# Kernel tuning notes

Hardware: AMD Instinct MI355X
Metric: run time of the kernel (lower is better)

## Reference

```python
import jax, jax.numpy as jnp
import numpy as np

B, S, D, H, FF = 16, 1024, 1024, 8, 4096
DH = D // H
EPS = 1e-5

def _ln(x, g, b):
    mu = jnp.mean(x, axis=-1, keepdims=True)
    var = jnp.mean((x - mu) ** 2, axis=-1, keepdims=True)
    return (x - mu) * jax.lax.rsqrt(var + EPS) * g + b

def setup_inputs() -> dict:
    key = jax.random.key(0)
    ks = jax.random.split(key, 12)
    sd = D ** -0.5
    return {
        "x": jax.random.normal(ks[0], (B, S, D), jnp.float32),
        "bias": jax.random.normal(ks[1], (S, S), jnp.float32),
        "Wq": jax.random.normal(ks[2], (D, D), jnp.float32) * sd,
        "bq": jnp.zeros((D,), jnp.float32),
        "Wk": jax.random.normal(ks[3], (D, D), jnp.float32) * sd,
        "bk": jnp.zeros((D,), jnp.float32),
        "Wv": jax.random.normal(ks[4], (D, D), jnp.float32) * sd,
        "bv": jnp.zeros((D,), jnp.float32),
        "Wo": jax.random.normal(ks[5], (D, D), jnp.float32) * sd,
        "bo": jnp.zeros((D,), jnp.float32),
        "ln1_g": jnp.ones((D,), jnp.float32),
        "ln1_b": jnp.zeros((D,), jnp.float32),
        "W1": jax.random.normal(ks[6], (FF, D), jnp.float32) * sd,
        "b1": jnp.zeros((FF,), jnp.float32),
        "W2": jax.random.normal(ks[7], (D, FF), jnp.float32) * (FF ** -0.5),
        "b2": jnp.zeros((D,), jnp.float32),
        "ln2_g": jnp.ones((D,), jnp.float32),
        "ln2_b": jnp.zeros((D,), jnp.float32),
    }

def reference(x, bias, Wq, bq, Wk, bk, Wv, bv, Wo, bo, ln1_g, ln1_b,
              W1, b1, W2, b2, ln2_g, ln2_b):
    # torch nn.Linear: y = x @ W.T + b
    Q = x @ Wq.T + bq  # [B,S,D]
    K = x @ Wk.T + bk
    V = x @ Wv.T + bv
    # Faithful to torch: plain row-major reshape [B,S,H*dh] -> [B*H,S,dh]
    Q = Q.reshape(B * H, S, DH)
    K = K.reshape(B * H, S, DH)
    V = V.reshape(B * H, S, DH)
    scale = DH ** -0.5
    scores = jnp.einsum('bqd,bkd->bqk', Q, K)  # [B*H,S,S]
    scores = (scores + bias[None]) * scale      # bias added BEFORE scaling, as in source
    attn = jax.nn.softmax(scores, axis=-1)
    selfattention = attn[0]
    ctx = jnp.einsum('bqk,bkd->bqd', attn, V).reshape(B, S, D)
    out = ctx @ Wo.T + bo
    out = _ln(out + x, ln1_g, ln1_b)
    # FFN
    h = jax.nn.relu(out @ W1.T + b1)
    ff = h @ W2.T + b2
    out2 = _ln(ff + out, ln2_g, ln2_b)
    return out2, selfattention
```

## Files before the change

### kernel.cpp

```cpp
#include <hip/hip_runtime.h>
#include <hip/hip_bf16.h>
#include <math.h>

typedef __attribute__((ext_vector_type(4))) float f32x4;
typedef __attribute__((ext_vector_type(8))) __bf16 bf16x8;
typedef __attribute__((ext_vector_type(4))) __bf16 bf16x4;

static constexpr float SCALE = 0.08838834764831845f;

__device__ __forceinline__ void load_lds16(const void* g, void* l) {
  __builtin_amdgcn_global_load_lds(
      (const __attribute__((address_space(1))) void*)g,
      (__attribute__((address_space(3))) void*)l, 16, 0, 0);
}

__global__ __launch_bounds__(256) void cast_kernel(const float* __restrict__ s,
                                                   __bf16* __restrict__ d, int n4) {
  int i = blockIdx.x * blockDim.x + threadIdx.x;
  int stride = gridDim.x * blockDim.x;
  for (; i < n4; i += stride) {
    float4 v = reinterpret_cast<const float4*>(s)[i];
    bf16x4 o;
    o[0] = (__bf16)v.x; o[1] = (__bf16)v.y; o[2] = (__bf16)v.z; o[3] = (__bf16)v.w;
    reinterpret_cast<bf16x4*>(d)[i] = o;
  }
}

__global__ __launch_bounds__(256) void transpose_bias(const float* __restrict__ src,
                                                      __bf16* __restrict__ dst) {
  __shared__ float tile[64][65];
  const int bx = blockIdx.x & 15;
  const int by = blockIdx.x >> 4;
  const int t = threadIdx.x;
  const int lx = t & 63, ly = t >> 6;
#pragma unroll
  for (int i = 0; i < 16; ++i) {
    int row = (ly << 4) + i;
    tile[row][lx] = src[(size_t)(by * 64 + row) * 1024 + bx * 64 + lx];
  }
  __syncthreads();
#pragma unroll
  for (int i = 0; i < 16; ++i) {
    int row = (ly << 4) + i;
    dst[(size_t)(bx * 64 + row) * 1024 + by * 64 + lx] = (__bf16)tile[lx][row];
  }
}

template <int EPI>
__global__ __launch_bounds__(512, 2) void gemm_bt(
    const __bf16* __restrict__ A, const __bf16* __restrict__ Bw,
    const float* __restrict__ bvec, __bf16* __restrict__ Cb,
    float* __restrict__ Cf, int M, int N, int K) {
  __shared__ __align__(16) char sm[131072];

  const int ntn = N >> 8;
  const int nwg = gridDim.x;
  const int bid = blockIdx.x;
  const int b = (bid & 7) * (nwg >> 3) + (bid >> 3);
  const int tm = b / ntn, tn = b % ntn;
  const int t = threadIdx.x, lane = t & 63;
  const int w = t >> 6;
  const int wm = w >> 2, wn = w & 3;
  const int l15 = lane & 15, lq = lane >> 4;

  f32x4 acc[8][4] = {};

  const int r0 = t >> 3;
  const int r1 = r0 + 64;
  const int kb0 = (((t & 7) << 4) ^ ((r0 & 7) << 4));
  const int wbase = w << 10;

  auto stage = [&](int kt, int p) {
    char* base = sm + (p << 16);
    const size_t kofs = (size_t)(kb0 >> 1) + ((size_t)kt << 6);
#pragma unroll
    for (int h = 0; h < 2; ++h) {
      const __bf16* gA = A + (size_t)((tm << 8) + (h << 7) + r0) * K + kofs;
      const __bf16* gA2 = A + (size_t)((tm << 8) + (h << 7) + r1) * K + kofs;
      char* lA = base + (h << 14) + wbase;
      load_lds16(gA, lA);
      load_lds16(gA2, lA + 8192);
      const __bf16* gB = Bw + (size_t)((tn << 8) + (h << 7) + r0) * K + kofs;
      const __bf16* gB2 = Bw + (size_t)((tn << 8) + (h << 7) + r1) * K + kofs;
      char* lB = base + 32768 + (h << 14) + wbase;
      load_lds16(gB, lB);
      load_lds16(gB2, lB + 8192);
    }
  };

  stage(0, 0);
  __syncthreads();

  const int NT = K >> 6;
  const int rbB = (wn & 1) << 6;
  for (int kt = 0; kt < NT; ++kt) {
    const int p = kt & 1;
    const char* Ab = sm + (p << 16) + (wm << 14);
    const char* Bb = sm + (p << 16) + 32768 + ((wn >> 1) << 14);
    if (kt + 1 < NT) stage(kt + 1, p ^ 1);

    bf16x8 bfv[4][2];
#pragma unroll
    for (int nf = 0; nf < 4; ++nf) {
      const int r = rbB + (nf << 4) + l15;
      const int sw = (r & 7) << 4;
#pragma unroll
      for (int ks = 0; ks < 2; ++ks) {
        const int lb = (ks << 6) + (lq << 4);
        bfv[nf][ks] = *(const bf16x8*)(Bb + r * 128 + (lb ^ sw));
      }
    }
#pragma unroll
    for (int q = 0; q < 4; ++q) {
      bf16x8 af[2][2];
#pragma unroll
      for (int dm = 0; dm < 2; ++dm) {
        const int r = (((q << 1) + dm) << 4) + l15;
        const int sw = (r & 7) << 4;
#pragma unroll
        for (int ks = 0; ks < 2; ++ks) {
          const int lb = (ks << 6) + (lq << 4);
          af[dm][ks] = *(const bf16x8*)(Ab + r * 128 + (lb ^ sw));
        }
      }
#pragma unroll
      for (int ks = 0; ks < 2; ++ks)
#pragma unroll
        for (int dm = 0; dm < 2; ++dm)
#pragma unroll
          for (int nf = 0; nf < 4; ++nf)
            acc[(q << 1) + dm][nf] = __builtin_amdgcn_mfma_f32_16x16x32_bf16(
                af[dm][ks], bfv[nf][ks], acc[(q << 1) + dm][nf], 0, 0, 0);
    }
    __syncthreads();
  }

  const int row0 = (tm << 8) + (wm << 7) + (lq << 2);
  const int col0 = (tn << 8) + (wn << 6) + l15;
#pragma unroll
  for (int nf = 0; nf < 4; ++nf) {
    const int col = col0 + (nf << 4);
    const float bv = bvec[col];
#pragma unroll
    for (int mf = 0; mf < 8; ++mf) {
#pragma unroll
      for (int r = 0; r < 4; ++r) {
        const int row = row0 + (mf << 4) + r;
        float v = acc[mf][nf][r] + bv;
        if (EPI == 1) v = fmaxf(v, 0.f);
        if (EPI == 2) {
          Cf[(size_t)row * N + col] = v;
        } else if (EPI == 3) {
          size_t vt = ((size_t)(row >> 7) << 17) + ((size_t)(col & 127) << 10) +
                      ((row & 127) << 3) + (col >> 7);
          Cb[vt] = (__bf16)v;
        } else {
          Cb[(size_t)row * N + col] = (__bf16)v;
        }
      }
    }
  }
}

__global__ __launch_bounds__(256) void attn_flash(
    const __bf16* __restrict__ Q, const __bf16* __restrict__ K,
    const __bf16* __restrict__ VT, const __bf16* __restrict__ biasT,
    __bf16* __restrict__ ctx) {
  __shared__ __bf16 Qs[64 * 128];
  __shared__ __bf16 Ks[64 * 128];
  __shared__ __bf16 VTs[128 * 64];
  __shared__ __bf16 Ps[4][16 * 64];

  const int bid = blockIdx.x;
  const int b = ((bid & 7) << 8) | (bid >> 3);
  const int g = b >> 4;
  const int q0 = (b & 15) << 6;
  const size_t goff = (size_t)g << 17;
  const __bf16* Qg = Q + goff;
  const __bf16* Kg = K + goff;
  const __bf16* VTg = VT + goff;

  const int t = threadIdx.x, w = t >> 6, lane = t & 63;
  const int l15 = lane & 15, lq = lane >> 4;

  {
    int srow = lane >> 4;
    int sbo = (lane & 15) << 4;
#pragma unroll
    for (int i = 0; i < 4; ++i) {
      int c = (w << 2) + i;
      int r = (c << 2) + srow;
      int ke = (sbo ^ ((r & 7) << 4)) >> 1;
      load_lds16(Qg + (size_t)(q0 + r) * 128 + ke, (char*)Qs + (c << 10));
    }
  }

  float mrun = -INFINITY, lrun = 0.f;
  f32x4 cacc[8] = {};
  bf16x8 qf[4];
  const int qg = q0 + (w << 4) + l15;
  const int ra = (w << 4) + l15;

  for (int kb = 0; kb < 1024; kb += 64) {
    {
      int srow = lane >> 4;
      int sbo = (lane & 15) << 4;
#pragma unroll
      for (int i = 0; i < 4; ++i) {
        int c = (w << 2) + i;
        int r = (c << 2) + srow;
        int ke = (sbo ^ ((r & 7) << 4)) >> 1;
        load_lds16(Kg + (size_t)(kb + r) * 128 + ke, (char*)Ks + (c << 10));
      }
    }
    {
      int srow = lane >> 3;
      int sbo = (lane & 7) << 4;
#pragma unroll
      for (int i = 0; i < 4; ++i) {
        int c = (w << 2) + i;
        int e = (c << 3) + srow;
        int ke = kb + ((sbo ^ ((e & 7) << 4)) >> 1);
        load_lds16(VTg + (size_t)e * 1024 + ke, (char*)VTs + (c << 10));
      }
    }
    __syncthreads();

    if (kb == 0) {
#pragma unroll
      for (int ec = 0; ec < 4; ++ec) {
        int lb = (ec << 6) + (lq << 4);
        qf[ec] = *(const bf16x8*)((const char*)Qs + ra * 256 + (lb ^ ((ra & 7) << 4)));
      }
    }

    f32x4 sacc[4] = {};
#pragma unroll
    for (int ec = 0; ec < 4; ++ec) {
      const int lb = (ec << 6) + (lq << 4);
#pragma unroll
      for (int kn = 0; kn < 4; ++kn) {
        int rb = (kn << 4) + l15;
        bf16x8 kf = *(const bf16x8*)((const char*)Ks + rb * 256 + (lb ^ ((rb & 7) << 4)));
        sacc[kn] = __builtin_amdgcn_mfma_f32_16x16x32_bf16(kf, qf[ec], sacc[kn], 0, 0, 0);
      }
    }

    float sv[4][4];
#pragma unroll
    for (int kn = 0; kn < 4; ++kn) {
      int kbase = kb + (kn << 4) + (lq << 2);
#pragma unroll
      for (int r = 0; r < 4; ++r)
        sv[kn][r] = (sacc[kn][r] + (float)biasT[((size_t)(kbase + r) << 10) + qg]) * SCALE;
    }
    float mt = sv[0][0];
#pragma unroll
    for (int kn = 0; kn < 4; ++kn)
#pragma unroll
      for (int r = 0; r < 4; ++r) mt = fmaxf(mt, sv[kn][r]);
    mt = fmaxf(mt, __shfl_xor(mt, 16));
    mt = fmaxf(mt, __shfl_xor(mt, 32));
    float mnew = fmaxf(mrun, mt);
    float alpha = __expf(mrun - mnew);
    mrun = mnew;
    float psum = 0.f;
#pragma unroll
    for (int kn = 0; kn < 4; ++kn)
#pragma unroll
      for (int r = 0; r < 4; ++r) {
        float p = __expf(sv[kn][r] - mnew);
        sv[kn][r] = p;
        psum += p;
      }
    psum += __shfl_xor(psum, 16);
    psum += __shfl_xor(psum, 32);
    lrun = lrun * alpha + psum;

    float alphaR[4];
#pragma unroll
    for (int r = 0; r < 4; ++r)
      alphaR[r] = __shfl(alpha, (lane & 48) + ((lane & 48) >> 2) + r);
#pragma unroll
    for (int et = 0; et < 8; ++et)
#pragma unroll
      for (int r = 0; r < 4; ++r) cacc[et][r] *= alphaR[r];

#pragma unroll
    for (int kn = 0; kn < 4; ++kn) {
      bf16x4 pk;
      pk[0] = (__bf16)sv[kn][0]; pk[1] = (__bf16)sv[kn][1];
      pk[2] = (__bf16)sv[kn][2]; pk[3] = (__bf16)sv[kn][3];
      int bo = (kn << 5) + (lq << 3);
      *(bf16x4*)((char*)Ps[w] + l15 * 128 + (bo ^ ((l15 & 7) << 4))) = pk;
    }
    asm volatile("s_waitcnt lgkmcnt(0)" ::: "memory");
    __builtin_amdgcn_sched_barrier(0);

#pragma unroll
    for (int ks = 0; ks < 2; ++ks) {
      const int lb = (ks << 6) + (lq << 4);
      bf16x8 paf = *(const bf16x8*)((const char*)Ps[w] + l15 * 128 + (lb ^ ((l15 & 7) << 4)));
#pragma unroll
      for (int et = 0; et < 8; ++et) {
        int e = (et << 4) + l15;
        bf16x8 vf = *(const bf16x8*)((const char*)VTs + e * 128 + (lb ^ ((e & 7) << 4)));
        cacc[et] = __builtin_amdgcn_mfma_f32_16x16x32_bf16(paf, vf, cacc[et], 0, 0, 0);
      }
    }
    __syncthreads();
  }

  float lrunR[4];
#pragma unroll
  for (int r = 0; r < 4; ++r)
    lrunR[r] = __shfl(lrun, (lane & 48) + ((lane & 48) >> 2) + r);
  __bf16* cg = ctx + goff;
  const int qr = q0 + (w << 4) + (lq << 2);
#pragma unroll
  for (int et = 0; et < 8; ++et)
#pragma unroll
    for (int r = 0; r < 4; ++r) {
      float v = cacc[et][r] / lrunR[r];
      cg[(size_t)(qr + r) * 128 + (et << 4) + l15] = (__bf16)v;
    }
}

__global__ __launch_bounds__(256) void attn_head0(
    const __bf16* __restrict__ Q, const __bf16* __restrict__ K,
    const float* __restrict__ bias, float* __restrict__ out) {
  __shared__ float qrow[128];
  __shared__ float red[8];
  const int q = blockIdx.x, t = threadIdx.x;
  if (t < 128) qrow[t] = (float)Q[(size_t)q * 128 + t];
  __syncthreads();
  float s[4];
#pragma unroll
  for (int c = 0; c < 4; ++c) {
    int kc = (c << 8) + t;
    const __bf16* kr = K + (size_t)kc * 128;
    float dot = 0.f;
#pragma unroll
    for (int e = 0; e < 128; e += 8) {
      bf16x8 kv = *(const bf16x8*)(kr + e);
#pragma unroll
      for (int j = 0; j < 8; ++j) dot += qrow[e + j] * (float)kv[j];
    }
    s[c] = (dot + bias[(size_t)q * 1024 + kc]) * SCALE;
  }
  float mx = fmaxf(fmaxf(s[0], s[1]), fmaxf(s[2], s[3]));
#pragma unroll
  for (int d = 32; d >= 1; d >>= 1) mx = fmaxf(mx, __shfl_xor(mx, d));
  const int w = t >> 6, lane = t & 63;
  if (lane == 0) red[w] = mx;
  __syncthreads();
  mx = fmaxf(fmaxf(red[0], red[1]), fmaxf(red[2], red[3]));
  float ex[4], sum = 0.f;
#pragma unroll
  for (int c = 0; c < 4; ++c) { ex[c] = __expf(s[c] - mx); sum += ex[c]; }
#pragma unroll
  for (int d = 32; d >= 1; d >>= 1) sum += __shfl_xor(sum, d);
  __syncthreads();
  if (lane == 0) red[4 + w] = sum;
  __syncthreads();
  sum = red[4] + red[5] + red[6] + red[7];
  float inv = 1.f / sum;
#pragma unroll
  for (int c = 0; c < 4; ++c) out[(size_t)q * 1024 + (c << 8) + t] = ex[c] * inv;
}

template <int B_BF16>
__global__ __launch_bounds__(256) void ln_res(
    const float* __restrict__ a, const void* __restrict__ bptr,
    const float* __restrict__ gam, const float* __restrict__ bet,
    float* __restrict__ outf, __bf16* __restrict__ outb) {
  __shared__ float red[8];
  const int row = blockIdx.x, t = threadIdx.x;
  const size_t base = (size_t)row << 10;
  float4 va = reinterpret_cast<const float4*>(a + base)[t];
  float b0, b1, b2, b3;
  if (B_BF16) {
    bf16x4 vb = reinterpret_cast<const bf16x4*>((const __bf16*)bptr + base)[t];
    b0 = (float)vb[0]; b1 = (float)vb[1]; b2 = (float)vb[2]; b3 = (float)vb[3];
  } else {
    float4 vb = reinterpret_cast<const float4*>((const float*)bptr + base)[t];
    b0 = vb.x; b1 = vb.y; b2 = vb.z; b3 = vb.w;
  }
  float v0 = va.x + b0, v1 = va.y + b1, v2 = va.z + b2, v3 = va.w + b3;
  float s = v0 + v1 + v2 + v3;
  float qq = v0 * v0 + v1 * v1 + v2 * v2 + v3 * v3;
#pragma unroll
  for (int d = 32; d >= 1; d >>= 1) {
    s += __shfl_xor(s, d);
    qq += __shfl_xor(qq, d);
  }
  const int w = t >> 6, lane = t & 63;
  if (lane == 0) { red[w] = s; red[4 + w] = qq; }
  __syncthreads();
  s = red[0] + red[1] + red[2] + red[3];
  qq = red[4] + red[5] + red[6] + red[7];
  const float mu = s * (1.f / 1024.f);
  const float var = qq * (1.f / 1024.f) - mu * mu;
  const float rs = rsqrtf(var + 1e-5f);
  float4 g4 = reinterpret_cast<const float4*>(gam)[t];
  float4 b4 = reinterpret_cast<const float4*>(bet)[t];
  float o0 = (v0 - mu) * rs * g4.x + b4.x;
  float o1 = (v1 - mu) * rs * g4.y + b4.y;
  float o2 = (v2 - mu) * rs * g4.z + b4.z;
  float o3 = (v3 - mu) * rs * g4.w + b4.w;
  if (outf) reinterpret_cast<float4*>(outf + base)[t] = make_float4(o0, o1, o2, o3);
  if (outb) {
    bf16x4 ob;
    ob[0] = (__bf16)o0; ob[1] = (__bf16)o1; ob[2] = (__bf16)o2; ob[3] = (__bf16)o3;
    reinterpret_cast<bf16x4*>(outb + base)[t] = ob;
  }
}

extern "C" void kernel_launch(void* const* d_in, const int* in_sizes, int n_in,
                              void* d_out, int out_size, void* d_ws, size_t ws_size,
                              hipStream_t stream) {
  (void)in_sizes; (void)n_in; (void)out_size; (void)ws_size;
  const float* x    = (const float*)d_in[0];
  const float* bias = (const float*)d_in[1];
  const float* Wq   = (const float*)d_in[2];
  const float* bq   = (const float*)d_in[3];
  const float* Wk   = (const float*)d_in[4];
  const float* bk   = (const float*)d_in[5];
  const float* Wv   = (const float*)d_in[6];
  const float* bv   = (const float*)d_in[7];
  const float* Wo   = (const float*)d_in[8];
  const float* bo   = (const float*)d_in[9];
  const float* g1   = (const float*)d_in[10];
  const float* b1l  = (const float*)d_in[11];
  const float* W1   = (const float*)d_in[12];
  const float* b1f  = (const float*)d_in[13];
  const float* W2   = (const float*)d_in[14];
  const float* b2f  = (const float*)d_in[15];
  const float* g2   = (const float*)d_in[16];
  const float* b2l  = (const float*)d_in[17];

  char* ws = (char*)d_ws;
  size_t off = 0;
  auto alloc = [&](size_t bytes) {
    char* p = ws + off;
    off += (bytes + 255) & ~(size_t)255;
    return p;
  };
  __bf16* wqb  = (__bf16*)alloc(2097152);
  __bf16* wkb  = (__bf16*)alloc(2097152);
  __bf16* wvb  = (__bf16*)alloc(2097152);
  __bf16* wob  = (__bf16*)alloc(2097152);
  __bf16* w1b  = (__bf16*)alloc(8388608);
  __bf16* w2b  = (__bf16*)alloc(8388608);
  __bf16* biasTb = (__bf16*)alloc(2097152);
  __bf16* xb   = (__bf16*)alloc(33554432);
  __bf16* Qb   = (__bf16*)alloc(4ull * 33554432);
  __bf16* Kb   = Qb + 16777216;
  __bf16* VTb  = Kb + 16777216;
  __bf16* ctxb = VTb + 16777216;
  __bf16* hb   = Qb;
  __bf16* res1b = xb;

  float* out2     = (float*)d_out;
  float* selfattn = (float*)d_out + 16777216;
  float* attn_out = out2;
  float* ff       = out2;

  cast_kernel<<<2048, 256, 0, stream>>>(x, xb, 16777216 / 4);
  cast_kernel<<<1024, 256, 0, stream>>>(Wq, wqb, 1048576 / 4);
  cast_kernel<<<1024, 256, 0, stream>>>(Wk, wkb, 1048576 / 4);
  cast_kernel<<<1024, 256, 0, stream>>>(Wv, wvb, 1048576 / 4);
  cast_kernel<<<1024, 256, 0, stream>>>(Wo, wob, 1048576 / 4);
  cast_kernel<<<1024, 256, 0, stream>>>(W1, w1b, 4194304 / 4);
  cast_kernel<<<1024, 256, 0, stream>>>(W2, w2b, 4194304 / 4);
  transpose_bias<<<256, 256, 0, stream>>>(bias, biasTb);

  gemm_bt<0><<<64 * 4, 512, 0, stream>>>(xb, wqb, bq, Qb, nullptr, 16384, 1024, 1024);
  gemm_bt<0><<<64 * 4, 512, 0, stream>>>(xb, wkb, bk, Kb, nullptr, 16384, 1024, 1024);
  gemm_bt<3><<<64 * 4, 512, 0, stream>>>(xb, wvb, bv, VTb, nullptr, 16384, 1024, 1024);

  attn_head0<<<1024, 256, 0, stream>>>(Qb, Kb, bias, selfattn);
  attn_flash<<<128 * 16, 256, 0, stream>>>(Qb, Kb, VTb, biasTb, ctxb);

  gemm_bt<2><<<64 * 4, 512, 0, stream>>>(ctxb, wob, bo, nullptr, attn_out, 16384, 1024, 1024);

  ln_res<0><<<16384, 256, 0, stream>>>(attn_out, x, g1, b1l, nullptr, res1b);

  gemm_bt<1><<<64 * 16, 512, 0, stream>>>(res1b, w1b, b1f, hb, nullptr, 16384, 4096, 1024);
  gemm_bt<2><<<64 * 4, 512, 0, stream>>>(hb, w2b, b2f, nullptr, ff, 16384, 1024, 4096);

  ln_res<1><<<16384, 256, 0, stream>>>(ff, res1b, g2, b2l, out2, nullptr);
}
```

Measured before the change: 773.2 us.

## Prescale bias into log2 domain, skip rescale when max unchanged, load Q directly

The bias transpose is replaced by a cast that premultiplies the bias by scale*log2e. Attention scores are then computed with one fma and exp2 instead of an add, a multiply and expf, and bias is read as contiguous bf16x4 rows rather than strided transposed scalars. Q fragments are loaded straight from global memory instead of staged through LDS. The accumulator rescale is skipped when no lane's running max grows, and s_setprio is raised around the MFMA blocks. The conditional rescale adds wave divergence checks, and rounding the prescaled bias to bf16 changes precision slightly.

```diff
diff --git a/kernel.cpp b/kernel.cpp
--- a/kernel.cpp
+++ b/kernel.cpp
@@ -7,6 +7,7 @@
 typedef __attribute__((ext_vector_type(4))) __bf16 bf16x4;
 
 static constexpr float SCALE = 0.08838834764831845f;
+static constexpr float SCALE_LOG2E = 0.1275174482f;
 
 __device__ __forceinline__ void load_lds16(const void* g, void* l) {
   __builtin_amdgcn_global_load_lds(
@@ -26,23 +27,16 @@
   }
 }
 
-__global__ __launch_bounds__(256) void transpose_bias(const float* __restrict__ src,
-                                                      __bf16* __restrict__ dst) {
-  __shared__ float tile[64][65];
-  const int bx = blockIdx.x & 15;
-  const int by = blockIdx.x >> 4;
-  const int t = threadIdx.x;
-  const int lx = t & 63, ly = t >> 6;
-#pragma unroll
-  for (int i = 0; i < 16; ++i) {
-    int row = (ly << 4) + i;
-    tile[row][lx] = src[(size_t)(by * 64 + row) * 1024 + bx * 64 + lx];
-  }
-  __syncthreads();
-#pragma unroll
-  for (int i = 0; i < 16; ++i) {
-    int row = (ly << 4) + i;
-    dst[(size_t)(bx * 64 + row) * 1024 + by * 64 + lx] = (__bf16)tile[lx][row];
+__global__ __launch_bounds__(256) void scale_cast_kernel(const float* __restrict__ s,
+                                                         __bf16* __restrict__ d, int n4) {
+  int i = blockIdx.x * blockDim.x + threadIdx.x;
+  int stride = gridDim.x * blockDim.x;
+  for (; i < n4; i += stride) {
+    float4 v = reinterpret_cast<const float4*>(s)[i];
+    bf16x4 o;
+    o[0] = (__bf16)(v.x * SCALE_LOG2E); o[1] = (__bf16)(v.y * SCALE_LOG2E);
+    o[2] = (__bf16)(v.z * SCALE_LOG2E); o[3] = (__bf16)(v.w * SCALE_LOG2E);
+    reinterpret_cast<bf16x4*>(d)[i] = o;
   }
 }
 
@@ -164,9 +158,8 @@
 
 __global__ __launch_bounds__(256) void attn_flash(
     const __bf16* __restrict__ Q, const __bf16* __restrict__ K,
-    const __bf16* __restrict__ VT, const __bf16* __restrict__ biasT,
+    const __bf16* __restrict__ VT, const __bf16* __restrict__ biasS,
     __bf16* __restrict__ ctx) {
-  __shared__ __bf16 Qs[64 * 128];
   __shared__ __bf16 Ks[64 * 128];
   __shared__ __bf16 VTs[128 * 64];
   __shared__ __bf16 Ps[4][16 * 64];
@@ -182,24 +175,18 @@
 
   const int t = threadIdx.x, w = t >> 6, lane = t & 63;
   const int l15 = lane & 15, lq = lane >> 4;
-
+  const int qg = q0 + (w << 4) + l15;
+
+  bf16x8 qf[4];
   {
-    int srow = lane >> 4;
-    int sbo = (lane & 15) << 4;
-#pragma unroll
-    for (int i = 0; i < 4; ++i) {
-      int c = (w << 2) + i;
-      int r = (c << 2) + srow;
-      int ke = (sbo ^ ((r & 7) << 4)) >> 1;
-      load_lds16(Qg + (size_t)(q0 + r) * 128 + ke, (char*)Qs + (c << 10));
-    }
-  }
+    const __bf16* qrow = Qg + (size_t)qg * 128 + (lq << 3);
+#pragma unroll
+    for (int ec = 0; ec < 4; ++ec) qf[ec] = *(const bf16x8*)(qrow + (ec << 5));
+  }
+  const __bf16* bSr = biasS + ((size_t)qg << 10) + (lq << 2);
 
   float mrun = -INFINITY, lrun = 0.f;
   f32x4 cacc[8] = {};
-  bf16x8 qf[4];
-  const int qg = q0 + (w << 4) + l15;
-  const int ra = (w << 4) + l15;
 
   for (int kb = 0; kb < 1024; kb += 64) {
     {
@@ -226,15 +213,8 @@
     }
     __syncthreads();
 
-    if (kb == 0) {
-#pragma unroll
-      for (int ec = 0; ec < 4; ++ec) {
-        int lb = (ec << 6) + (lq << 4);
-        qf[ec] = *(const bf16x8*)((const char*)Qs + ra * 256 + (lb ^ ((ra & 7) << 4)));
-      }
-    }
-
     f32x4 sacc[4] = {};
+    __builtin_amdgcn_s_setprio(1);
 #pragma unroll
     for (int ec = 0; ec < 4; ++ec) {
       const int lb = (ec << 6) + (lq << 4);
@@ -245,14 +225,16 @@
         sacc[kn] = __builtin_amdgcn_mfma_f32_16x16x32_bf16(kf, qf[ec], sacc[kn], 0, 0, 0);
       }
     }
+    __builtin_amdgcn_s_setprio(0);
 
     float sv[4][4];
+    const __bf16* bt = bSr + kb;
 #pragma unroll
     for (int kn = 0; kn < 4; ++kn) {
-      int kbase = kb + (kn << 4) + (lq << 2);
+      bf16x4 bb = *(const bf16x4*)(bt + (kn << 4));
 #pragma unroll
       for (int r = 0; r < 4; ++r)
-        sv[kn][r] = (sacc[kn][r] + (float)biasT[((size_t)(kbase + r) << 10) + qg]) * SCALE;
+        sv[kn][r] = fmaf(sacc[kn][r], SCALE_LOG2E, (float)bb[r]);
     }
     float mt = sv[0][0];
 #pragma unroll
@@ -261,30 +243,33 @@
       for (int r = 0; r < 4; ++r) mt = fmaxf(mt, sv[kn][r]);
     mt = fmaxf(mt, __shfl_xor(mt, 16));
     mt = fmaxf(mt, __shfl_xor(mt, 32));
-    float mnew = fmaxf(mrun, mt);
-    float alpha = __expf(mrun - mnew);
-    mrun = mnew;
+
+    float alpha = 1.f;
+    if (__any(mt > mrun)) {
+      float mnew = fmaxf(mrun, mt);
+      alpha = exp2f(mrun - mnew);
+      mrun = mnew;
+      float alphaR[4];
+#pragma unroll
+      for (int r = 0; r < 4; ++r)
+        alphaR[r] = __shfl(alpha, (lane & 48) + ((lane & 48) >> 2) + r);
+#pragma unroll
+      for (int et = 0; et < 8; ++et)
+#pragma unroll
+        for (int r = 0; r < 4; ++r) cacc[et][r] *= alphaR[r];
+    }
     float psum = 0.f;
 #pragma unroll
     for (int kn = 0; kn < 4; ++kn)
 #pragma unroll
       for (int r = 0; r < 4; ++r) {
-        float p = __expf(sv[kn][r] - mnew);
+        float p = exp2f(sv[kn][r] - mrun);
         sv[kn][r] = p;
         psum += p;
       }
     psum += __shfl_xor(psum, 16);
     psum += __shfl_xor(psum, 32);
     lrun = lrun * alpha + psum;
-
-    float alphaR[4];
-#pragma unroll
-    for (int r = 0; r < 4; ++r)
-      alphaR[r] = __shfl(alpha, (lane & 48) + ((lane & 48) >> 2) + r);
-#pragma unroll
-    for (int et = 0; et < 8; ++et)
-#pragma unroll
-      for (int r = 0; r < 4; ++r) cacc[et][r] *= alphaR[r];
 
 #pragma unroll
     for (int kn = 0; kn < 4; ++kn) {
@@ -297,6 +282,7 @@
     asm volatile("s_waitcnt lgkmcnt(0)" ::: "memory");
     __builtin_amdgcn_sched_barrier(0);
 
+    __builtin_amdgcn_s_setprio(1);
 #pragma unroll
     for (int ks = 0; ks < 2; ++ks) {
       const int lb = (ks << 6) + (lq << 4);
@@ -308,6 +294,7 @@
         cacc[et] = __builtin_amdgcn_mfma_f32_16x16x32_bf16(paf, vf, cacc[et], 0, 0, 0);
       }
     }
+    __builtin_amdgcn_s_setprio(0);
     __syncthreads();
   }
 
@@ -452,7 +439,7 @@
   __bf16* wob  = (__bf16*)alloc(2097152);
   __bf16* w1b  = (__bf16*)alloc(8388608);
   __bf16* w2b  = (__bf16*)alloc(8388608);
-  __bf16* biasTb = (__bf16*)alloc(2097152);
+  __bf16* biasS = (__bf16*)alloc(2097152);
   __bf16* xb   = (__bf16*)alloc(33554432);
   __bf16* Qb   = (__bf16*)alloc(4ull * 33554432);
   __bf16* Kb   = Qb + 16777216;
@@ -473,14 +460,14 @@
   cast_kernel<<<1024, 256, 0, stream>>>(Wo, wob, 1048576 / 4);
   cast_kernel<<<1024, 256, 0, stream>>>(W1, w1b, 4194304 / 4);
   cast_kernel<<<1024, 256, 0, stream>>>(W2, w2b, 4194304 / 4);
-  transpose_bias<<<256, 256, 0, stream>>>(bias, biasTb);
+  scale_cast_kernel<<<512, 256, 0, stream>>>(bias, biasS, 1048576 / 4);
 
   gemm_bt<0><<<64 * 4, 512, 0, stream>>>(xb, wqb, bq, Qb, nullptr, 16384, 1024, 1024);
   gemm_bt<0><<<64 * 4, 512, 0, stream>>>(xb, wkb, bk, Kb, nullptr, 16384, 1024, 1024);
   gemm_bt<3><<<64 * 4, 512, 0, stream>>>(xb, wvb, bv, VTb, nullptr, 16384, 1024, 1024);
 
   attn_head0<<<1024, 256, 0, stream>>>(Qb, Kb, bias, selfattn);
-  attn_flash<<<128 * 16, 256, 0, stream>>>(Qb, Kb, VTb, biasTb, ctxb);
+  attn_flash<<<128 * 16, 256, 0, stream>>>(Qb, Kb, VTb, biasS, ctxb);
 
   gemm_bt<2><<<64 * 4, 512, 0, stream>>>(ctxb, wob, bo, nullptr, attn_out, 16384, 1024, 1024);
 
```

Measured after the change: 779.9 us. About the same (+0.9%).
